# Performance work log

Measured on AMD Instinct MI355X. Metric: run time of the kernel, lower is better.

## Reference

```python
import jax, jax.numpy as jnp
import numpy as np

H = 512      # hidden_size
L = 32       # label_size
P = 1024     # number_of_persons
N = 16385    # events per sequence (n-1 = 16384 recurrent steps)
M = 16384    # simulated integration points
NUM_EQ = 7
TARGET = 1


def setup_inputs() -> dict:
    key = jax.random.key(0)
    ks = jax.random.split(key, 10)
    label_seq = jax.random.randint(ks[0], (N,), 0, L + 1)
    dt = jax.random.uniform(ks[1], (N,), jnp.float32, 1e-3, 1.0)
    time_seq = jnp.cumsum(dt)                       # strictly increasing
    sim_time_idx = jax.random.randint(ks[2], (M,), 0, N - 1)
    u = jax.random.uniform(ks[3], (M,), jnp.float32)
    # sim time lies inside interval [t_idx, t_idx+1]
    sim_time_seq = time_seq[sim_time_idx] + u * (time_seq[sim_time_idx + 1] - time_seq[sim_time_idx])
    def uni(k, shape):
        stdv = 1.0 / np.sqrt(shape[-1])
        return jax.random.uniform(k, shape, jnp.float32, -stdv, stdv)
    Emb = uni(ks[4], (H, L + 1))
    EmbPersonalised = uni(ks[5], (H, P))
    W = uni(ks[6], (NUM_EQ, H, H))
    U = uni(ks[7], (NUM_EQ, H, H))
    d = jnp.zeros((NUM_EQ, H), jnp.float32)
    w = uni(ks[8], (L, H))
    log_s = jnp.zeros((L,), jnp.float32)
    return {"label_seq": label_seq, "time_seq": time_seq, "sim_time_seq": sim_time_seq,
            "sim_time_idx": sim_time_idx, "seq_id": 7,
            "Emb": Emb, "EmbPersonalised": EmbPersonalised, "W": W, "U": U,
            "d": d, "w": w, "log_s": log_s}


def _h_to_lambd(h, w, log_s):
    s = jnp.exp(log_s)                               # [L]
    lambd_tilda = h @ w.T                            # [..., L]
    return s * jax.nn.softplus(lambd_tilda / s) + 1e-9


def reference(label_seq, time_seq, sim_time_seq, sim_time_idx, seq_id,
              Emb, EmbPersonalised, W, U, d, w, log_s):
    labels = Emb[:, label_seq].T                     # [N, H] event embeddings
    pers = EmbPersonalised[:, seq_id]                # [H]
    # label_prev at step i (i=1..N-1): pers for i=1, else Emb[:, label_seq[i-1]]
    prev_lab = jnp.concatenate([pers[None, :], labels[1:-1]], axis=0)  # [N-1, H]
    t_prev = time_seq[:-1]
    t_cur = time_seq[1:]

    def step(carry, x):
        c_t, h_t, c_bar = carry
        lab, tp, tc = x
        temp = jnp.einsum('eij,j->ei', W, lab) + jnp.einsum('eij,j->ei', U, h_t) + d  # [7, H]
        i_g = jax.nn.sigmoid(temp[0])
        f_g = jax.nn.sigmoid(temp[1])
        z = jnp.tanh(temp[2])
        o = jax.nn.sigmoid(temp[3])
        i2 = jax.nn.sigmoid(temp[4])
        f2 = jax.nn.sigmoid(temp[5])
        delta = jax.nn.softplus(temp[6])
        c = f_g * c_t + i_g * z
        c_bar = f2 * c_bar + i2 * z
        c_t = c_bar + (c - c_bar) * jnp.exp(-delta * (tc - tp))
        h_t = o * jnp.tanh(c_t)
        return (c_t, h_t, c_bar), (h_t, c_bar, c, delta, o)

    zeros = jnp.zeros((H,), jnp.float32)
    init = (zeros, zeros, zeros)
    _, (all_h, all_cb, all_c, all_delta, all_o) = jax.lax.scan(
        step, init, (prev_lab, t_prev, t_cur))      # each [N-1, H]

    # term1: log-intensity at observed target events
    h_obs = all_h[:-1]                               # [N-2, H]
    lambd = _h_to_lambd(h_obs, w, log_s)             # [N-2, L]
    mask = label_seq[1:-1] == TARGET
    term1 = jnp.sum(jnp.where(mask, jnp.log(lambd[:, TARGET - 1]), 0.0))

    # term2: Monte-Carlo integral of target intensity
    dt_sim = (sim_time_seq - time_seq[sim_time_idx])[:, None]  # [M, 1]
    c_sim = all_cb[sim_time_idx] + (all_c[sim_time_idx] - all_cb[sim_time_idx]) * \
        jnp.exp(-all_delta[sim_time_idx] * dt_sim)
    h_sim = all_o[sim_time_idx] * jnp.tanh(c_sim)
    lambd_sim = _h_to_lambd(h_sim, w, log_s)
    term2 = jnp.mean(lambd_sim[:, TARGET - 1]) * (time_seq[-1] - time_seq[0])

    return -(term1 - term2)
```

## Files before the change

kernel.cpp:

```cpp
#include <hip/hip_runtime.h>
#include <math.h>

#define NLAB   33
#define HD     512
#define NEQ    7
#define NSEQ   16385
#define TSTEPS 16384
#define MSIM   16384
#define GWG    32
#define CH     16
#define RROWS  (NEQ*CH)
#define BTHR   512
#define NB1    4096
#define NB2    4096
#define CANARY 0xFFFFFFFFu

__device__ __forceinline__ float sigmoid_(float x) { return 1.0f / (1.0f + __expf(-x)); }
__device__ __forceinline__ float softplus_(float x) { return fmaxf(x, 0.0f) + log1pf(__expf(-fabsf(x))); }
__device__ __forceinline__ float tanh_(float x) {
  float ax = fabsf(x);
  float e  = __expf(2.0f * ax);
  float t  = 1.0f - 2.0f / (e + 1.0f);
  return copysignf(t, x);
}

__global__ void precompute_kernel(const float* __restrict__ W,
                                  const float* __restrict__ Emb,
                                  const float* __restrict__ EmbP,
                                  const int*   __restrict__ seq_id,
                                  float* __restrict__ WEmb,
                                  float* __restrict__ WPers) {
  int idx = blockIdx.x * blockDim.x + threadIdx.x;
  const int total = NEQ * HD * (NLAB + 1);
  if (idx >= total) return;
  int l  = idx % (NLAB + 1);
  int ij = idx / (NLAB + 1);
  const float* Wrow = W + (size_t)ij * HD;
  float acc = 0.0f;
  if (l < NLAB) {
    for (int k = 0; k < HD; ++k) acc = fmaf(Wrow[k], Emb[(size_t)k * NLAB + l], acc);
    WEmb[(size_t)ij * NLAB + l] = acc;
  } else {
    int sid = seq_id[0];
    for (int k = 0; k < HD; ++k) acc = fmaf(Wrow[k], EmbP[(size_t)k * 1024 + sid], acc);
    WPers[ij] = acc;
  }
}

__global__ __launch_bounds__(BTHR, 1) void scan_kernel(
    const int*   __restrict__ label_seq,
    const float* __restrict__ time_seq,
    const float* __restrict__ U,
    const float* __restrict__ dvec,
    const float* __restrict__ WEmb,
    const float* __restrict__ WPers,
    float* __restrict__ h_hist,
    float* __restrict__ c_hist,
    float* __restrict__ cb_hist,
    float* __restrict__ dl_hist,
    float* __restrict__ o_hist) {
  const int g   = blockIdx.x;
  const int tid = threadIdx.x;
  const int kg  = tid & 7;
  const int rs  = tid >> 3;

  const int  r0  = rs;
  const int  r1  = rs + 64;
  const bool v1  = (r1 < RROWS);
  const int  e0  = r0 / CH, jj0 = r0 % CH;
  const int  e1  = v1 ? (r1 / CH) : 0, jj1 = v1 ? (r1 % CH) : 0;
  const int  jg0 = g * CH + jj0, jg1 = g * CH + jj1;

  float u0[64], u1[64];
  {
    const float* Ur0 = U + ((size_t)e0 * HD + jg0) * HD + kg * 64;
    const float* Ur1 = U + ((size_t)e1 * HD + jg1) * HD + kg * 64;
#pragma unroll
    for (int b = 0; b < 16; ++b) {
      int cb = ((b + kg) & 15) * 4;
      float4 a = *(const float4*)(Ur0 + cb);
      u0[4*b+0] = a.x; u0[4*b+1] = a.y; u0[4*b+2] = a.z; u0[4*b+3] = a.w;
      float4 c = *(const float4*)(Ur1 + cb);
      u1[4*b+0] = c.x; u1[4*b+1] = c.y; u1[4*b+2] = c.z; u1[4*b+3] = c.w;
    }
  }
  const float d0 = dvec[e0 * HD + jg0];
  const float d1 = dvec[e1 * HD + jg1];

  __shared__ float h_lds[HD];
  __shared__ float temp_lds[NEQ][CH];
  __shared__ float wemb_lds[RROWS * NLAB];
  for (int idx = tid; idx < RROWS * NLAB; idx += BTHR) {
    int rr = idx / NLAB, l = idx % NLAB;
    int e = rr / CH, jj = rr % CH;
    wemb_lds[idx] = WEmb[((size_t)e * HD + g * CH + jj) * NLAB + l];
  }

  float c_reg = 0.0f, cb_reg = 0.0f;
  float hreg[64];
#pragma unroll
  for (int kk = 0; kk < 64; ++kk) hreg[kk] = 0.0f;
  __syncthreads();

  for (int t = 0; t < TSTEPS; ++t) {
    float wl0 = 0.0f, wl1 = 0.0f;
    if (kg == 0) {
      if (t > 0) {
        int lab = label_seq[t];
        wl0 = wemb_lds[r0 * NLAB + lab];
        if (v1) wl1 = wemb_lds[r1 * NLAB + lab];
      } else {
        wl0 = WPers[e0 * HD + jg0];
        if (v1) wl1 = WPers[e1 * HD + jg1];
      }
    }
    float tp = 0.0f, tc = 0.0f;
    if (tid < CH) { tp = time_seq[t]; tc = time_seq[t + 1]; }

    float acc0 = 0.0f, acc1 = 0.0f;
#pragma unroll
    for (int kk = 0; kk < 64; ++kk) {
      acc0 = fmaf(u0[kk], hreg[kk], acc0);
      acc1 = fmaf(u1[kk], hreg[kk], acc1);
    }
#pragma unroll
    for (int m = 1; m <= 4; m <<= 1) {
      acc0 += __shfl_xor(acc0, m, 64);
      acc1 += __shfl_xor(acc1, m, 64);
    }
    if (kg == 0) {
      temp_lds[e0][jj0] = acc0 + d0 + wl0;
      if (v1) temp_lds[e1][jj1] = acc1 + d1 + wl1;
    }
    __syncthreads();

    if (tid < 64) {
      if (tid < CH) {
        int j = tid, jgl = g * CH + j;
        float i_g = sigmoid_(temp_lds[0][j]);
        float f_g = sigmoid_(temp_lds[1][j]);
        float z   = tanh_(temp_lds[2][j]);
        float o   = sigmoid_(temp_lds[3][j]);
        float i2  = sigmoid_(temp_lds[4][j]);
        float f2  = sigmoid_(temp_lds[5][j]);
        float dl  = softplus_(temp_lds[6][j]);
        float cn  = f_g * c_reg + i_g * z;
        float cbn = f2 * cb_reg + i2 * z;
        float ef  = __expf(-dl * (tc - tp));
        float cd  = cbn + (cn - cbn) * ef;
        float h   = o * tanh_(cd);
        c_reg  = cd;
        cb_reg = cbn;
        size_t off = (size_t)t * HD + jgl;
        __hip_atomic_store((unsigned*)&h_hist[off], __float_as_uint(h),
                           __ATOMIC_RELAXED, __HIP_MEMORY_SCOPE_AGENT);
        c_hist[off]  = cn;
        cb_hist[off] = cbn;
        dl_hist[off] = dl;
        o_hist[off]  = o;
      }
      if (t + 1 < TSTEPS) {
        const unsigned* mb = (const unsigned*)(h_hist + (size_t)t * HD);
        unsigned v[8];
        bool ok;
        do {
#pragma unroll
          for (int i = 0; i < 8; ++i)
            v[i] = __hip_atomic_load(&mb[tid * 8 + i], __ATOMIC_RELAXED, __HIP_MEMORY_SCOPE_AGENT);
          ok = true;
#pragma unroll
          for (int i = 0; i < 8; ++i) ok = ok && (v[i] != CANARY);
        } while (!ok);
#pragma unroll
        for (int i = 0; i < 8; ++i) h_lds[tid * 8 + i] = __uint_as_float(v[i]);
      }
    }
    __syncthreads();

    if (t + 1 < TSTEPS) {
#pragma unroll
      for (int b = 0; b < 16; ++b) {
        int cb = ((b + kg) & 15) * 4;
        float4 v = *(const float4*)&h_lds[kg * 64 + cb];
        hreg[4*b+0] = v.x; hreg[4*b+1] = v.y; hreg[4*b+2] = v.z; hreg[4*b+3] = v.w;
      }
    }
  }
}

__global__ void term1_kernel(const float* __restrict__ h_hist,
                             const float* __restrict__ wmat,
                             const int*   __restrict__ label_seq,
                             const float* __restrict__ log_s,
                             float* __restrict__ partial1) {
  int wid  = (blockIdx.x * blockDim.x + threadIdx.x) >> 6;
  int lane = threadIdx.x & 63;
  float lsum = 0.0f;
  if (wid < TSTEPS - 1) {
    const float* hr = h_hist + (size_t)wid * HD;
    float acc = 0.0f;
#pragma unroll
    for (int i = 0; i < 8; ++i) acc = fmaf(hr[lane * 8 + i], wmat[lane * 8 + i], acc);
#pragma unroll
    for (int m = 1; m < 64; m <<= 1) acc += __shfl_xor(acc, m, 64);
    if (lane == 0 && label_seq[wid + 1] == 1) {
      float s0  = __expf(log_s[0]);
      float lam = s0 * softplus_(acc / s0) + 1e-9f;
      lsum = __logf(lam);
    }
  }
  __shared__ float bsum[4];
  if (lane == 0) bsum[threadIdx.x >> 6] = lsum;
  __syncthreads();
  if (threadIdx.x == 0) partial1[blockIdx.x] = bsum[0] + bsum[1] + bsum[2] + bsum[3];
}

__global__ void term2_kernel(const float* __restrict__ c_hist,
                             const float* __restrict__ cb_hist,
                             const float* __restrict__ dl_hist,
                             const float* __restrict__ o_hist,
                             const float* __restrict__ wmat,
                             const float* __restrict__ log_s,
                             const int*   __restrict__ sim_idx,
                             const float* __restrict__ sim_time,
                             const float* __restrict__ time_seq,
                             float* __restrict__ partial2) {
  int wid  = (blockIdx.x * blockDim.x + threadIdx.x) >> 6;
  int lane = threadIdx.x & 63;
  float lsum = 0.0f;
  if (wid < MSIM) {
    int   idx = sim_idx[wid];
    float dts = sim_time[wid] - time_seq[idx];
    size_t off = (size_t)idx * HD + lane * 8;
    float acc = 0.0f;
#pragma unroll
    for (int i = 0; i < 8; ++i) {
      float cb = cb_hist[off + i];
      float c  = c_hist[off + i];
      float dl = dl_hist[off + i];
      float o  = o_hist[off + i];
      float cs = cb + (c - cb) * __expf(-dl * dts);
      float hs = o * tanh_(cs);
      acc = fmaf(hs, wmat[lane * 8 + i], acc);
    }
#pragma unroll
    for (int m = 1; m < 64; m <<= 1) acc += __shfl_xor(acc, m, 64);
    if (lane == 0) {
      float s0 = __expf(log_s[0]);
      lsum = s0 * softplus_(acc / s0) + 1e-9f;
    }
  }
  __shared__ float bsum[4];
  if (lane == 0) bsum[threadIdx.x >> 6] = lsum;
  __syncthreads();
  if (threadIdx.x == 0) partial2[blockIdx.x] = bsum[0] + bsum[1] + bsum[2] + bsum[3];
}

__global__ void final_kernel(const float* __restrict__ partial1,
                             const float* __restrict__ partial2,
                             const float* __restrict__ time_seq,
                             float* __restrict__ out) {
  int lane = threadIdx.x;
  float s1 = 0.0f, s2 = 0.0f;
  for (int i = lane; i < NB1; i += 64) s1 += partial1[i];
  for (int i = lane; i < NB2; i += 64) s2 += partial2[i];
#pragma unroll
  for (int m = 1; m < 64; m <<= 1) {
    s1 += __shfl_xor(s1, m, 64);
    s2 += __shfl_xor(s2, m, 64);
  }
  if (lane == 0) {
    float term1 = s1;
    float term2 = (s2 / (float)MSIM) * (time_seq[NSEQ - 1] - time_seq[0]);
    out[0] = -(term1 - term2);
  }
}

extern "C" void kernel_launch(void* const* d_in, const int* in_sizes, int n_in,
                              void* d_out, int out_size, void* d_ws, size_t ws_size,
                              hipStream_t stream) {
  const int*   label_seq = (const int*)  d_in[0];
  const float* time_seq  = (const float*)d_in[1];
  const float* sim_time  = (const float*)d_in[2];
  const int*   sim_idx   = (const int*)  d_in[3];
  const int*   seq_id    = (const int*)  d_in[4];
  const float* Emb       = (const float*)d_in[5];
  const float* EmbP      = (const float*)d_in[6];
  const float* W         = (const float*)d_in[7];
  const float* U         = (const float*)d_in[8];
  const float* dvec      = (const float*)d_in[9];
  const float* wmat      = (const float*)d_in[10];
  const float* log_s     = (const float*)d_in[11];
  float* out = (float*)d_out;

  char* ws = (char*)d_ws;
  size_t off = 0;
  auto alloc = [&](size_t bytes) -> void* {
    void* p = ws + off;
    off += (bytes + 255) & ~(size_t)255;
    return p;
  };
  float*    WEmb     = (float*)   alloc((size_t)NEQ * HD * NLAB * 4);
  float*    WPers    = (float*)   alloc((size_t)NEQ * HD * 4);
  float*    h_hist   = (float*)   alloc((size_t)TSTEPS * HD * 4);
  float*    c_hist   = (float*)   alloc((size_t)TSTEPS * HD * 4);
  float*    cb_hist  = (float*)   alloc((size_t)TSTEPS * HD * 4);
  float*    dl_hist  = (float*)   alloc((size_t)TSTEPS * HD * 4);
  float*    o_hist   = (float*)   alloc((size_t)TSTEPS * HD * 4);
  float*    partial1 = (float*)   alloc((size_t)NB1 * 4);
  float*    partial2 = (float*)   alloc((size_t)NB2 * 4);
  (void)ws_size; (void)in_sizes; (void)n_in; (void)out_size;

  hipMemsetAsync(h_hist, 0xFF, (size_t)TSTEPS * HD * 4, stream);

  {
    int total  = NEQ * HD * (NLAB + 1);
    int blocks = (total + 255) / 256;
    precompute_kernel<<<blocks, 256, 0, stream>>>(W, Emb, EmbP, seq_id, WEmb, WPers);
  }
  scan_kernel<<<GWG, BTHR, 0, stream>>>(label_seq, time_seq, U, dvec, WEmb, WPers,
                                        h_hist, c_hist, cb_hist, dl_hist, o_hist);
  term1_kernel<<<NB1, 256, 0, stream>>>(h_hist, wmat, label_seq, log_s, partial1);
  term2_kernel<<<NB2, 256, 0, stream>>>(c_hist, cb_hist, dl_hist, o_hist, wmat, log_s,
                                        sim_idx, sim_time, time_seq, partial2);
  final_kernel<<<1, 64, 0, stream>>>(partial1, partial2, time_seq, out);
}
```

Measured before the change: 43.01 ms.

## Exchange hidden state through small ring mailbox instead of full history buffer

Cross-block exchange of each step's hidden state now goes through a 4-slot mailbox ring that stays hot in cache, rather than polling the full h_hist array. A second wavefront handles the polling, reading with 64-bit atomics, while each block writes its own slice directly into LDS and resets the slot from two steps earlier to the canary. History stores become nontemporal, and the large memset of h_hist is replaced by a small mailbox memset. The intent is lower per-step synchronisation latency on the serial recurrence. The cost is more complex slot-recycling logic that must stay race-free.

After: 41.81 ms. 2.8% less time.

```diff
diff --git a/kernel.cpp b/kernel.cpp
--- a/kernel.cpp
+++ b/kernel.cpp
@@ -11,6 +11,7 @@
 #define CH     16
 #define RROWS  (NEQ*CH)
 #define BTHR   512
+#define SLOTS  4
 #define NB1    4096
 #define NB2    4096
 #define CANARY 0xFFFFFFFFu
@@ -54,6 +55,7 @@
     const float* __restrict__ dvec,
     const float* __restrict__ WEmb,
     const float* __restrict__ WPers,
+    float* __restrict__ mbox,
     float* __restrict__ h_hist,
     float* __restrict__ c_hist,
     float* __restrict__ cb_hist,
@@ -133,6 +135,9 @@
       if (v1) temp_lds[e1][jj1] = acc1 + d1 + wl1;
     }
     __syncthreads();
+
+    const int slot = t & (SLOTS - 1);
+    float* mrow = mbox + slot * HD;
 
     if (tid < 64) {
       if (tid < CH) {
@@ -151,28 +156,45 @@
         float h   = o * tanh_(cd);
         c_reg  = cd;
         cb_reg = cbn;
+        h_lds[jgl] = h;
+        __hip_atomic_store((unsigned*)&mrow[jgl], __float_as_uint(h),
+                           __ATOMIC_RELAXED, __HIP_MEMORY_SCOPE_AGENT);
         size_t off = (size_t)t * HD + jgl;
-        __hip_atomic_store((unsigned*)&h_hist[off], __float_as_uint(h),
-                           __ATOMIC_RELAXED, __HIP_MEMORY_SCOPE_AGENT);
-        c_hist[off]  = cn;
-        cb_hist[off] = cbn;
-        dl_hist[off] = dl;
-        o_hist[off]  = o;
+        __builtin_nontemporal_store(h,   &h_hist[off]);
+        __builtin_nontemporal_store(cn,  &c_hist[off]);
+        __builtin_nontemporal_store(cbn, &cb_hist[off]);
+        __builtin_nontemporal_store(dl,  &dl_hist[off]);
+        __builtin_nontemporal_store(o,   &o_hist[off]);
       }
-      if (t + 1 < TSTEPS) {
-        const unsigned* mb = (const unsigned*)(h_hist + (size_t)t * HD);
-        unsigned v[8];
+    } else if (tid < 128 && t + 1 < TSTEPS) {
+      const int lane = tid - 64;
+      if ((lane >> 1) == g) {
+        if (t >= 2) {
+          unsigned long long* dead =
+              (unsigned long long*)(mbox + ((t - 2) & (SLOTS - 1)) * HD + g * CH + (lane & 1) * 8);
+#pragma unroll
+          for (int i = 0; i < 4; ++i)
+            __hip_atomic_store(&dead[i], 0xFFFFFFFFFFFFFFFFull,
+                               __ATOMIC_RELAXED, __HIP_MEMORY_SCOPE_AGENT);
+        }
+      } else {
+        const unsigned long long* mb = (const unsigned long long*)(mrow + lane * 8);
+        unsigned long long q[4];
         bool ok;
         do {
 #pragma unroll
-          for (int i = 0; i < 8; ++i)
-            v[i] = __hip_atomic_load(&mb[tid * 8 + i], __ATOMIC_RELAXED, __HIP_MEMORY_SCOPE_AGENT);
+          for (int i = 0; i < 4; ++i)
+            q[i] = __hip_atomic_load(&mb[i], __ATOMIC_RELAXED, __HIP_MEMORY_SCOPE_AGENT);
           ok = true;
 #pragma unroll
-          for (int i = 0; i < 8; ++i) ok = ok && (v[i] != CANARY);
+          for (int i = 0; i < 4; ++i)
+            ok = ok && ((unsigned)q[i] != CANARY) && ((unsigned)(q[i] >> 32) != CANARY);
         } while (!ok);
 #pragma unroll
-        for (int i = 0; i < 8; ++i) h_lds[tid * 8 + i] = __uint_as_float(v[i]);
+        for (int i = 0; i < 4; ++i) {
+          h_lds[lane * 8 + 2*i + 0] = __uint_as_float((unsigned)q[i]);
+          h_lds[lane * 8 + 2*i + 1] = __uint_as_float((unsigned)(q[i] >> 32));
+        }
       }
     }
     __syncthreads();
@@ -302,6 +324,7 @@
   };
   float*    WEmb     = (float*)   alloc((size_t)NEQ * HD * NLAB * 4);
   float*    WPers    = (float*)   alloc((size_t)NEQ * HD * 4);
+  float*    mbox     = (float*)   alloc((size_t)SLOTS * HD * 4);
   float*    h_hist   = (float*)   alloc((size_t)TSTEPS * HD * 4);
   float*    c_hist   = (float*)   alloc((size_t)TSTEPS * HD * 4);
   float*    cb_hist  = (float*)   alloc((size_t)TSTEPS * HD * 4);
@@ -311,7 +334,7 @@
   float*    partial2 = (float*)   alloc((size_t)NB2 * 4);
   (void)ws_size; (void)in_sizes; (void)n_in; (void)out_size;
 
-  hipMemsetAsync(h_hist, 0xFF, (size_t)TSTEPS * HD * 4, stream);
+  hipMemsetAsync(mbox, 0xFF, (size_t)SLOTS * HD * 4, stream);
 
   {
     int total  = NEQ * HD * (NLAB + 1);
@@ -319,7 +342,7 @@
     precompute_kernel<<<blocks, 256, 0, stream>>>(W, Emb, EmbP, seq_id, WEmb, WPers);
   }
   scan_kernel<<<GWG, BTHR, 0, stream>>>(label_seq, time_seq, U, dvec, WEmb, WPers,
-                                        h_hist, c_hist, cb_hist, dl_hist, o_hist);
+                                        mbox, h_hist, c_hist, cb_hist, dl_hist, o_hist);
   term1_kernel<<<NB1, 256, 0, stream>>>(h_hist, wmat, label_seq, log_s, partial1);
   term2_kernel<<<NB2, 256, 0, stream>>>(c_hist, cb_hist, dl_hist, o_hist, wmat, log_s,
                                         sim_idx, sim_time, time_seq, partial2);
```

## Exchange hidden state via fp16 ring mailbox with dot2 recurrent matvec

Applied to the files above, without the earlier changes.

Packs U into fp16 pairs and computes the recurrent matvec with fdot2, which halves register footprint and the number of multiply instructions. The cross-workgroup h exchange moves from polling the full fp32 h_hist to a small 4-slot fp16 mailbox. A separate wavefront polls it with 64-bit loads and clears slots two steps back, so the memset shrinks and the poll traffic on the critical path is smaller. The cost is reduced precision in the recurrence over many steps and the added complexity of slot recycling.

Result: slower. 49.40 ms (+14.8%).

```diff
diff --git a/kernel.cpp b/kernel.cpp
--- a/kernel.cpp
+++ b/kernel.cpp
@@ -1,4 +1,5 @@
 #include <hip/hip_runtime.h>
+#include <hip/hip_fp16.h>
 #include <math.h>
 
 #define NLAB   33
@@ -11,9 +12,14 @@
 #define CH     16
 #define RROWS  (NEQ*CH)
 #define BTHR   512
+#define SLOTS  4
+#define MROW   256
 #define NB1    4096
 #define NB2    4096
 #define CANARY 0xFFFFFFFFu
+
+typedef _Float16 half2v __attribute__((ext_vector_type(2)));
+union h2cvt { unsigned u; half2v h; };
 
 __device__ __forceinline__ float sigmoid_(float x) { return 1.0f / (1.0f + __expf(-x)); }
 __device__ __forceinline__ float softplus_(float x) { return fmaxf(x, 0.0f) + log1pf(__expf(-fabsf(x))); }
@@ -22,6 +28,11 @@
   float e  = __expf(2.0f * ax);
   float t  = 1.0f - 2.0f / (e + 1.0f);
   return copysignf(t, x);
+}
+__device__ __forceinline__ unsigned pack2h(float a, float b) {
+  unsigned lo = (unsigned)__half_as_ushort(__float2half(a));
+  unsigned hi = (unsigned)__half_as_ushort(__float2half(b));
+  return lo | (hi << 16);
 }
 
 __global__ void precompute_kernel(const float* __restrict__ W,
@@ -47,13 +58,23 @@
   }
 }
 
+__global__ void packU_kernel(const float* __restrict__ U, unsigned* __restrict__ Upk) {
+  int idx = blockIdx.x * blockDim.x + threadIdx.x;
+  if (idx >= NEQ * HD * (HD / 2)) return;
+  int k2    = idx & 255;
+  int rowij = idx >> 8;
+  const float* r = U + (size_t)rowij * HD + 2 * k2;
+  Upk[idx] = pack2h(r[0], r[1]);
+}
+
 __global__ __launch_bounds__(BTHR, 1) void scan_kernel(
     const int*   __restrict__ label_seq,
     const float* __restrict__ time_seq,
-    const float* __restrict__ U,
+    const unsigned* __restrict__ Upk,
     const float* __restrict__ dvec,
     const float* __restrict__ WEmb,
     const float* __restrict__ WPers,
+    unsigned* __restrict__ mbox,
     float* __restrict__ h_hist,
     float* __restrict__ c_hist,
     float* __restrict__ cb_hist,
@@ -71,23 +92,23 @@
   const int  e1  = v1 ? (r1 / CH) : 0, jj1 = v1 ? (r1 % CH) : 0;
   const int  jg0 = g * CH + jj0, jg1 = g * CH + jj1;
 
-  float u0[64], u1[64];
+  unsigned u0[32], u1[32];
   {
-    const float* Ur0 = U + ((size_t)e0 * HD + jg0) * HD + kg * 64;
-    const float* Ur1 = U + ((size_t)e1 * HD + jg1) * HD + kg * 64;
-#pragma unroll
-    for (int b = 0; b < 16; ++b) {
-      int cb = ((b + kg) & 15) * 4;
-      float4 a = *(const float4*)(Ur0 + cb);
+    const uint4* Ur0 = (const uint4*)(Upk + (((size_t)e0 * HD + jg0) << 8));
+    const uint4* Ur1 = (const uint4*)(Upk + (((size_t)e1 * HD + jg1) << 8));
+#pragma unroll
+    for (int b = 0; b < 8; ++b) {
+      int cb = (b + kg) & 7;
+      uint4 a = Ur0[kg * 8 + cb];
       u0[4*b+0] = a.x; u0[4*b+1] = a.y; u0[4*b+2] = a.z; u0[4*b+3] = a.w;
-      float4 c = *(const float4*)(Ur1 + cb);
+      uint4 c = Ur1[kg * 8 + cb];
       u1[4*b+0] = c.x; u1[4*b+1] = c.y; u1[4*b+2] = c.z; u1[4*b+3] = c.w;
     }
   }
   const float d0 = dvec[e0 * HD + jg0];
   const float d1 = dvec[e1 * HD + jg1];
 
-  __shared__ float h_lds[HD];
+  __shared__ __align__(16) unsigned h16_lds[MROW];
   __shared__ float temp_lds[NEQ][CH];
   __shared__ float wemb_lds[RROWS * NLAB];
   for (int idx = tid; idx < RROWS * NLAB; idx += BTHR) {
@@ -97,9 +118,9 @@
   }
 
   float c_reg = 0.0f, cb_reg = 0.0f;
-  float hreg[64];
-#pragma unroll
-  for (int kk = 0; kk < 64; ++kk) hreg[kk] = 0.0f;
+  unsigned hreg[32];
+#pragma unroll
+  for (int kk = 0; kk < 32; ++kk) hreg[kk] = 0u;
   __syncthreads();
 
   for (int t = 0; t < TSTEPS; ++t) {
@@ -119,9 +140,10 @@
 
     float acc0 = 0.0f, acc1 = 0.0f;
 #pragma unroll
-    for (int kk = 0; kk < 64; ++kk) {
-      acc0 = fmaf(u0[kk], hreg[kk], acc0);
-      acc1 = fmaf(u1[kk], hreg[kk], acc1);
+    for (int kk = 0; kk < 32; ++kk) {
+      h2cvt ua{u0[kk]}, ub{u1[kk]}, hh{hreg[kk]};
+      acc0 = __builtin_amdgcn_fdot2(ua.h, hh.h, acc0, false);
+      acc1 = __builtin_amdgcn_fdot2(ub.h, hh.h, acc1, false);
     }
 #pragma unroll
     for (int m = 1; m <= 4; m <<= 1) {
@@ -133,6 +155,9 @@
       if (v1) temp_lds[e1][jj1] = acc1 + d1 + wl1;
     }
     __syncthreads();
+
+    const int slot = t & (SLOTS - 1);
+    unsigned* mrow = mbox + slot * MROW;
 
     if (tid < 64) {
       if (tid < CH) {
@@ -151,37 +176,60 @@
         float h   = o * tanh_(cd);
         c_reg  = cd;
         cb_reg = cbn;
+        float hn = __shfl_xor(h, 1, 64);
+        if ((j & 1) == 0) {
+          unsigned pk = pack2h(h, hn);
+          h16_lds[g * 8 + (j >> 1)] = pk;
+          __hip_atomic_store(&mrow[g * 8 + (j >> 1)], pk,
+                             __ATOMIC_RELAXED, __HIP_MEMORY_SCOPE_AGENT);
+        }
         size_t off = (size_t)t * HD + jgl;
-        __hip_atomic_store((unsigned*)&h_hist[off], __float_as_uint(h),
-                           __ATOMIC_RELAXED, __HIP_MEMORY_SCOPE_AGENT);
+        h_hist[off]  = h;
         c_hist[off]  = cn;
         cb_hist[off] = cbn;
         dl_hist[off] = dl;
         o_hist[off]  = o;
       }
-      if (t + 1 < TSTEPS) {
-        const unsigned* mb = (const unsigned*)(h_hist + (size_t)t * HD);
-        unsigned v[8];
-        bool ok;
-        do {
-#pragma unroll
-          for (int i = 0; i < 8; ++i)
-            v[i] = __hip_atomic_load(&mb[tid * 8 + i], __ATOMIC_RELAXED, __HIP_MEMORY_SCOPE_AGENT);
-          ok = true;
-#pragma unroll
-          for (int i = 0; i < 8; ++i) ok = ok && (v[i] != CANARY);
-        } while (!ok);
-#pragma unroll
-        for (int i = 0; i < 8; ++i) h_lds[tid * 8 + i] = __uint_as_float(v[i]);
+    } else if (tid < 128 && t + 1 < TSTEPS) {
+      const int L = tid - 64;
+      if ((L >> 1) == g) {
+        if (t >= 2) {
+          unsigned long long* dead =
+              (unsigned long long*)(mbox + ((t - 2) & (SLOTS - 1)) * MROW + 4 * L);
+          __hip_atomic_store(&dead[0], 0xFFFFFFFFFFFFFFFFull,
+                             __ATOMIC_RELAXED, __HIP_MEMORY_SCOPE_AGENT);
+          __hip_atomic_store(&dead[1], 0xFFFFFFFFFFFFFFFFull,
+                             __ATOMIC_RELAXED, __HIP_MEMORY_SCOPE_AGENT);
+        }
+      } else {
+        const unsigned long long* mb = (const unsigned long long*)(mrow + 4 * L);
+        auto okw = [](unsigned long long x) -> bool {
+          return (((unsigned)x != CANARY) & ((unsigned)(x >> 32) != CANARY));
+        };
+        unsigned long long r0v, r1v;
+        unsigned long long a0 = __hip_atomic_load(&mb[0], __ATOMIC_RELAXED, __HIP_MEMORY_SCOPE_AGENT);
+        unsigned long long a1 = __hip_atomic_load(&mb[1], __ATOMIC_RELAXED, __HIP_MEMORY_SCOPE_AGENT);
+        for (;;) {
+          unsigned long long b0 = __hip_atomic_load(&mb[0], __ATOMIC_RELAXED, __HIP_MEMORY_SCOPE_AGENT);
+          unsigned long long b1 = __hip_atomic_load(&mb[1], __ATOMIC_RELAXED, __HIP_MEMORY_SCOPE_AGENT);
+          if (okw(a0) & okw(a1)) { r0v = a0; r1v = a1; break; }
+          a0 = __hip_atomic_load(&mb[0], __ATOMIC_RELAXED, __HIP_MEMORY_SCOPE_AGENT);
+          a1 = __hip_atomic_load(&mb[1], __ATOMIC_RELAXED, __HIP_MEMORY_SCOPE_AGENT);
+          if (okw(b0) & okw(b1)) { r0v = b0; r1v = b1; break; }
+        }
+        unsigned long long* dst = (unsigned long long*)(h16_lds + 4 * L);
+        dst[0] = r0v;
+        dst[1] = r1v;
       }
     }
     __syncthreads();
 
     if (t + 1 < TSTEPS) {
-#pragma unroll
-      for (int b = 0; b < 16; ++b) {
-        int cb = ((b + kg) & 15) * 4;
-        float4 v = *(const float4*)&h_lds[kg * 64 + cb];
+      const uint4* hl4 = (const uint4*)h16_lds;
+#pragma unroll
+      for (int b = 0; b < 8; ++b) {
+        int cb = (b + kg) & 7;
+        uint4 v = hl4[kg * 8 + cb];
         hreg[4*b+0] = v.x; hreg[4*b+1] = v.y; hreg[4*b+2] = v.z; hreg[4*b+3] = v.w;
       }
     }
@@ -302,6 +350,8 @@
   };
   float*    WEmb     = (float*)   alloc((size_t)NEQ * HD * NLAB * 4);
   float*    WPers    = (float*)   alloc((size_t)NEQ * HD * 4);
+  unsigned* Upk      = (unsigned*)alloc((size_t)NEQ * HD * (HD / 2) * 4);
+  unsigned* mbox     = (unsigned*)alloc((size_t)SLOTS * MROW * 4);
   float*    h_hist   = (float*)   alloc((size_t)TSTEPS * HD * 4);
   float*    c_hist   = (float*)   alloc((size_t)TSTEPS * HD * 4);
   float*    cb_hist  = (float*)   alloc((size_t)TSTEPS * HD * 4);
@@ -311,15 +361,20 @@
   float*    partial2 = (float*)   alloc((size_t)NB2 * 4);
   (void)ws_size; (void)in_sizes; (void)n_in; (void)out_size;
 
-  hipMemsetAsync(h_hist, 0xFF, (size_t)TSTEPS * HD * 4, stream);
+  hipMemsetAsync(mbox, 0xFF, (size_t)SLOTS * MROW * 4, stream);
 
   {
     int total  = NEQ * HD * (NLAB + 1);
     int blocks = (total + 255) / 256;
     precompute_kernel<<<blocks, 256, 0, stream>>>(W, Emb, EmbP, seq_id, WEmb, WPers);
   }
-  scan_kernel<<<GWG, BTHR, 0, stream>>>(label_seq, time_seq, U, dvec, WEmb, WPers,
-                                        h_hist, c_hist, cb_hist, dl_hist, o_hist);
+  {
+    int total  = NEQ * HD * (HD / 2);
+    int blocks = (total + 255) / 256;
+    packU_kernel<<<blocks, 256, 0, stream>>>(U, Upk);
+  }
+  scan_kernel<<<GWG, BTHR, 0, stream>>>(label_seq, time_seq, Upk, dvec, WEmb, WPers,
+                                        mbox, h_hist, c_hist, cb_hist, dl_hist, o_hist);
   term1_kernel<<<NB1, 256, 0, stream>>>(h_hist, wmat, label_seq, log_s, partial1);
   term2_kernel<<<NB2, 256, 0, stream>>>(c_hist, cb_hist, dl_hist, o_hist, wmat, log_s,
                                         sim_idx, sim_time, time_seq, partial2);
```

## Use ring mailbox and per-wave gate math to cut one barrier per step

Applied to the files above, without the earlier changes.

The persistent scan kernel now exchanges hidden states through a small 4-slot ring mailbox instead of polling the full h_hist array. Each wave owns two output units across all seven gates, so gates are gathered with shuffles and the nonlinearities run redundantly in every lane, removing the second __syncthreads and the temp LDS round trip. The bias d is folded into WEmb/WPers at precompute, and mailbox loads are issued early to overlap with the matvec. It relies on careful slot reuse: slots are reset to the canary two steps later, which risks races if blocks drift more than the ring depth.

New measurement: 105.0 ms. +144.2%, slower.

```diff
diff --git a/kernel.cpp b/kernel.cpp
--- a/kernel.cpp
+++ b/kernel.cpp
@@ -9,8 +9,9 @@
 #define MSIM   16384
 #define GWG    32
 #define CH     16
-#define RROWS  (NEQ*CH)
 #define BTHR   512
+#define SLOTS  4
+#define WCOL   34
 #define NB1    4096
 #define NB2    4096
 #define CANARY 0xFFFFFFFFu
@@ -28,6 +29,7 @@
                                   const float* __restrict__ Emb,
                                   const float* __restrict__ EmbP,
                                   const int*   __restrict__ seq_id,
+                                  const float* __restrict__ dvec,
                                   float* __restrict__ WEmb,
                                   float* __restrict__ WPers) {
   int idx = blockIdx.x * blockDim.x + threadIdx.x;
@@ -36,7 +38,7 @@
   int l  = idx % (NLAB + 1);
   int ij = idx / (NLAB + 1);
   const float* Wrow = W + (size_t)ij * HD;
-  float acc = 0.0f;
+  float acc = dvec[ij];
   if (l < NLAB) {
     for (int k = 0; k < HD; ++k) acc = fmaf(Wrow[k], Emb[(size_t)k * NLAB + l], acc);
     WEmb[(size_t)ij * NLAB + l] = acc;
@@ -51,9 +53,9 @@
     const int*   __restrict__ label_seq,
     const float* __restrict__ time_seq,
     const float* __restrict__ U,
-    const float* __restrict__ dvec,
     const float* __restrict__ WEmb,
     const float* __restrict__ WPers,
+    float* __restrict__ mbox,
     float* __restrict__ h_hist,
     float* __restrict__ c_hist,
     float* __restrict__ cb_hist,
@@ -61,20 +63,19 @@
     float* __restrict__ o_hist) {
   const int g   = blockIdx.x;
   const int tid = threadIdx.x;
-  const int kg  = tid & 7;
-  const int rs  = tid >> 3;
-
-  const int  r0  = rs;
-  const int  r1  = rs + 64;
-  const bool v1  = (r1 < RROWS);
-  const int  e0  = r0 / CH, jj0 = r0 % CH;
-  const int  e1  = v1 ? (r1 / CH) : 0, jj1 = v1 ? (r1 % CH) : 0;
-  const int  jg0 = g * CH + jj0, jg1 = g * CH + jj1;
+  const int wv  = tid >> 6;
+  const int l   = tid & 63;
+  const int e   = l >> 3;
+  const int kg  = l & 7;
+  const int ee  = (e < 7) ? e : 6;
+
+  const int uA = 2 * wv, uB = 2 * wv + 1;
+  const int jA = g * CH + uA, jB = g * CH + uB;
 
   float u0[64], u1[64];
   {
-    const float* Ur0 = U + ((size_t)e0 * HD + jg0) * HD + kg * 64;
-    const float* Ur1 = U + ((size_t)e1 * HD + jg1) * HD + kg * 64;
+    const float* Ur0 = U + ((size_t)ee * HD + jA) * HD + kg * 64;
+    const float* Ur1 = U + ((size_t)ee * HD + jB) * HD + kg * 64;
 #pragma unroll
     for (int b = 0; b < 16; ++b) {
       int cb = ((b + kg) & 15) * 4;
@@ -84,38 +85,35 @@
       u1[4*b+0] = c.x; u1[4*b+1] = c.y; u1[4*b+2] = c.z; u1[4*b+3] = c.w;
     }
   }
-  const float d0 = dvec[e0 * HD + jg0];
-  const float d1 = dvec[e1 * HD + jg1];
 
   __shared__ float h_lds[HD];
-  __shared__ float temp_lds[NEQ][CH];
-  __shared__ float wemb_lds[RROWS * NLAB];
-  for (int idx = tid; idx < RROWS * NLAB; idx += BTHR) {
-    int rr = idx / NLAB, l = idx % NLAB;
-    int e = rr / CH, jj = rr % CH;
-    wemb_lds[idx] = WEmb[((size_t)e * HD + g * CH + jj) * NLAB + l];
-  }
-
-  float c_reg = 0.0f, cb_reg = 0.0f;
+  __shared__ float wemb_lds[NEQ * CH * WCOL];
+  for (int idx = tid; idx < NEQ * CH * WCOL; idx += BTHR) {
+    int r = idx / WCOL, c = idx % WCOL;
+    int re = r / CH, rj = r % CH;
+    int ij = re * HD + g * CH + rj;
+    wemb_lds[idx] = (c < NLAB) ? WEmb[(size_t)ij * NLAB + c] : WPers[ij];
+  }
+
+  float cA = 0.0f, cbA = 0.0f, cB = 0.0f, cbB = 0.0f;
   float hreg[64];
 #pragma unroll
   for (int kk = 0; kk < 64; ++kk) hreg[kk] = 0.0f;
+  float tp = time_seq[0];
   __syncthreads();
 
   for (int t = 0; t < TSTEPS; ++t) {
-    float wl0 = 0.0f, wl1 = 0.0f;
-    if (kg == 0) {
-      if (t > 0) {
-        int lab = label_seq[t];
-        wl0 = wemb_lds[r0 * NLAB + lab];
-        if (v1) wl1 = wemb_lds[r1 * NLAB + lab];
-      } else {
-        wl0 = WPers[e0 * HD + jg0];
-        if (v1) wl1 = WPers[e1 * HD + jg1];
-      }
-    }
-    float tp = 0.0f, tc = 0.0f;
-    if (tid < CH) { tp = time_seq[t]; tc = time_seq[t + 1]; }
+    const int slot = t & (SLOTS - 1);
+    float* mrow = mbox + slot * HD;
+    const bool more = (t + 1 < TSTEPS);
+    const bool own  = ((tid >> 4) == g);
+
+    unsigned pv = CANARY;
+    if (more && !own)
+      pv = __hip_atomic_load((const unsigned*)&mrow[tid], __ATOMIC_RELAXED, __HIP_MEMORY_SCOPE_AGENT);
+
+    const int lidx = (t > 0) ? label_seq[t] : NLAB;
+    const float tc = time_seq[t + 1];
 
     float acc0 = 0.0f, acc1 = 0.0f;
 #pragma unroll
@@ -128,56 +126,64 @@
       acc0 += __shfl_xor(acc0, m, 64);
       acc1 += __shfl_xor(acc1, m, 64);
     }
-    if (kg == 0) {
-      temp_lds[e0][jj0] = acc0 + d0 + wl0;
-      if (v1) temp_lds[e1][jj1] = acc1 + d1 + wl1;
+
+    float tAv[7], tBv[7];
+#pragma unroll
+    for (int q = 0; q < 7; ++q) {
+      float a = __shfl(acc0, q * 8, 64);
+      float b = __shfl(acc1, q * 8, 64);
+      tAv[q] = a + wemb_lds[(q * CH + uA) * WCOL + lidx];
+      tBv[q] = b + wemb_lds[(q * CH + uB) * WCOL + lidx];
+    }
+    const float dt = tc - tp;
+    float i_gA = sigmoid_(tAv[0]), f_gA = sigmoid_(tAv[1]), zA = tanh_(tAv[2]);
+    float oA = sigmoid_(tAv[3]), i2A = sigmoid_(tAv[4]), f2A = sigmoid_(tAv[5]);
+    float dlA = softplus_(tAv[6]);
+    float cnA  = f_gA * cA + i_gA * zA;
+    float cbnA = f2A * cbA + i2A * zA;
+    float cdA  = cbnA + (cnA - cbnA) * __expf(-dlA * dt);
+    float hA   = oA * tanh_(cdA);
+    cA = cdA; cbA = cbnA;
+    float i_gB = sigmoid_(tBv[0]), f_gB = sigmoid_(tBv[1]), zB = tanh_(tBv[2]);
+    float oB = sigmoid_(tBv[3]), i2B = sigmoid_(tBv[4]), f2B = sigmoid_(tBv[5]);
+    float dlB = softplus_(tBv[6]);
+    float cnB  = f_gB * cB + i_gB * zB;
+    float cbnB = f2B * cbB + i2B * zB;
+    float cdB  = cbnB + (cnB - cbnB) * __expf(-dlB * dt);
+    float hB   = oB * tanh_(cdB);
+    cB = cdB; cbB = cbnB;
+
+    if (l == 0) {
+      h_lds[jA] = hA;
+      __hip_atomic_store((unsigned*)&mrow[jA], __float_as_uint(hA),
+                         __ATOMIC_RELAXED, __HIP_MEMORY_SCOPE_AGENT);
+      size_t off = (size_t)t * HD + jA;
+      h_hist[off] = hA; c_hist[off] = cnA; cb_hist[off] = cbnA;
+      dl_hist[off] = dlA; o_hist[off] = oA;
+    } else if (l == 1) {
+      h_lds[jB] = hB;
+      __hip_atomic_store((unsigned*)&mrow[jB], __float_as_uint(hB),
+                         __ATOMIC_RELAXED, __HIP_MEMORY_SCOPE_AGENT);
+      size_t off = (size_t)t * HD + jB;
+      h_hist[off] = hB; c_hist[off] = cnB; cb_hist[off] = cbnB;
+      dl_hist[off] = dlB; o_hist[off] = oB;
+    }
+
+    if (more) {
+      if (own) {
+        if (t >= 2)
+          __hip_atomic_store((unsigned*)&mbox[((t - 2) & (SLOTS - 1)) * HD + tid], CANARY,
+                             __ATOMIC_RELAXED, __HIP_MEMORY_SCOPE_AGENT);
+      } else {
+        unsigned v = pv;
+        while (v == CANARY)
+          v = __hip_atomic_load((const unsigned*)&mrow[tid], __ATOMIC_RELAXED, __HIP_MEMORY_SCOPE_AGENT);
+        h_lds[tid] = __uint_as_float(v);
+      }
     }
     __syncthreads();
 
-    if (tid < 64) {
-      if (tid < CH) {
-        int j = tid, jgl = g * CH + j;
-        float i_g = sigmoid_(temp_lds[0][j]);
-        float f_g = sigmoid_(temp_lds[1][j]);
-        float z   = tanh_(temp_lds[2][j]);
-        float o   = sigmoid_(temp_lds[3][j]);
-        float i2  = sigmoid_(temp_lds[4][j]);
-        float f2  = sigmoid_(temp_lds[5][j]);
-        float dl  = softplus_(temp_lds[6][j]);
-        float cn  = f_g * c_reg + i_g * z;
-        float cbn = f2 * cb_reg + i2 * z;
-        float ef  = __expf(-dl * (tc - tp));
-        float cd  = cbn + (cn - cbn) * ef;
-        float h   = o * tanh_(cd);
-        c_reg  = cd;
-        cb_reg = cbn;
-        size_t off = (size_t)t * HD + jgl;
-        __hip_atomic_store((unsigned*)&h_hist[off], __float_as_uint(h),
-                           __ATOMIC_RELAXED, __HIP_MEMORY_SCOPE_AGENT);
-        c_hist[off]  = cn;
-        cb_hist[off] = cbn;
-        dl_hist[off] = dl;
-        o_hist[off]  = o;
-      }
-      if (t + 1 < TSTEPS) {
-        const unsigned* mb = (const unsigned*)(h_hist + (size_t)t * HD);
-        unsigned v[8];
-        bool ok;
-        do {
-#pragma unroll
-          for (int i = 0; i < 8; ++i)
-            v[i] = __hip_atomic_load(&mb[tid * 8 + i], __ATOMIC_RELAXED, __HIP_MEMORY_SCOPE_AGENT);
-          ok = true;
-#pragma unroll
-          for (int i = 0; i < 8; ++i) ok = ok && (v[i] != CANARY);
-        } while (!ok);
-#pragma unroll
-        for (int i = 0; i < 8; ++i) h_lds[tid * 8 + i] = __uint_as_float(v[i]);
-      }
-    }
-    __syncthreads();
-
-    if (t + 1 < TSTEPS) {
+    if (more) {
 #pragma unroll
       for (int b = 0; b < 16; ++b) {
         int cb = ((b + kg) & 15) * 4;
@@ -185,6 +191,7 @@
         hreg[4*b+0] = v.x; hreg[4*b+1] = v.y; hreg[4*b+2] = v.z; hreg[4*b+3] = v.w;
       }
     }
+    tp = tc;
   }
 }
 
@@ -302,6 +309,7 @@
   };
   float*    WEmb     = (float*)   alloc((size_t)NEQ * HD * NLAB * 4);
   float*    WPers    = (float*)   alloc((size_t)NEQ * HD * 4);
+  float*    mbox     = (float*)   alloc((size_t)SLOTS * HD * 4);
   float*    h_hist   = (float*)   alloc((size_t)TSTEPS * HD * 4);
   float*    c_hist   = (float*)   alloc((size_t)TSTEPS * HD * 4);
   float*    cb_hist  = (float*)   alloc((size_t)TSTEPS * HD * 4);
@@ -311,15 +319,15 @@
   float*    partial2 = (float*)   alloc((size_t)NB2 * 4);
   (void)ws_size; (void)in_sizes; (void)n_in; (void)out_size;
 
-  hipMemsetAsync(h_hist, 0xFF, (size_t)TSTEPS * HD * 4, stream);
+  hipMemsetAsync(mbox, 0xFF, (size_t)SLOTS * HD * 4, stream);
 
   {
     int total  = NEQ * HD * (NLAB + 1);
     int blocks = (total + 255) / 256;
-    precompute_kernel<<<blocks, 256, 0, stream>>>(W, Emb, EmbP, seq_id, WEmb, WPers);
-  }
-  scan_kernel<<<GWG, BTHR, 0, stream>>>(label_seq, time_seq, U, dvec, WEmb, WPers,
-                                        h_hist, c_hist, cb_hist, dl_hist, o_hist);
+    precompute_kernel<<<blocks, 256, 0, stream>>>(W, Emb, EmbP, seq_id, dvec, WEmb, WPers);
+  }
+  scan_kernel<<<GWG, BTHR, 0, stream>>>(label_seq, time_seq, U, WEmb, WPers,
+                                        mbox, h_hist, c_hist, cb_hist, dl_hist, o_hist);
   term1_kernel<<<NB1, 256, 0, stream>>>(h_hist, wmat, label_seq, log_s, partial1);
   term2_kernel<<<NB2, 256, 0, stream>>>(c_hist, cb_hist, dl_hist, o_hist, wmat, log_s,
                                         sim_idx, sim_time, time_seq, partial2);
```
